# Kernel optimization log

Hardware: AMD Instinct MI355X
Metric: run time of the kernel (lower is better)

The kernel has to match this reference:

```python
import jax, jax.numpy as jnp
import numpy as np

N_NODES = 50000
N_EDGES = 800000
D_IN = 128
HC = 128
D_OUT = 128
BN_EPS = 1e-5
RRELU_SLOPE = (1.0 / 8.0 + 1.0 / 3.0) / 2.0  # RReLU eval mode: (lower+upper)/2 = 11/48


def setup_inputs() -> dict:
    key = jax.random.key(0)
    ks = jax.random.split(key, 10)
    s_in = 1.0 / np.sqrt(D_IN)
    s_hc = 1.0 / np.sqrt(HC)
    return {
        "x": jax.random.normal(ks[0], (N_NODES, D_IN), jnp.float32),
        "edge_index": jax.random.randint(ks[1], (2, N_EDGES), 0, N_NODES),
        "edge_attr": jax.random.uniform(ks[2], (N_EDGES,), jnp.float32),
        # conv1: GraphConv(D_IN -> HC): lin_rel (with bias) + lin_root (no bias)
        "W1_rel": jax.random.normal(ks[3], (HC, D_IN), jnp.float32) * s_in,
        "b1": jnp.zeros((HC,), jnp.float32),
        "W1_root": jax.random.normal(ks[4], (HC, D_IN), jnp.float32) * s_in,
        # bn1 affine params
        "gamma": jnp.ones((HC,), jnp.float32),
        "beta": jnp.zeros((HC,), jnp.float32),
        # conv2: GraphConv(HC -> D_OUT)
        "W2_rel": jax.random.normal(ks[5], (D_OUT, HC), jnp.float32) * s_hc,
        "b2": jnp.zeros((D_OUT,), jnp.float32),
        "W2_root": jax.random.normal(ks[6], (D_OUT, HC), jnp.float32) * s_hc,
    }


def graph_conv(x, src, tgt, edge_w, W_rel, b_rel, W_root):
    # message: edge_weight * x[src]; aggregate: scatter-add into target nodes
    msg = x[src] * edge_w[:, None]                                   # [E, F]
    agg = jax.ops.segment_sum(msg, tgt, num_segments=x.shape[0])     # [N, F]
    return agg @ W_rel.T + b_rel + x @ W_root.T                      # [N, F_out]


def reference(x, edge_index, edge_attr, W1_rel, b1, W1_root, gamma, beta, W2_rel, b2, W2_root):
    src, tgt = edge_index[0], edge_index[1]
    h = graph_conv(x, src, tgt, edge_attr, W1_rel, b1, W1_root)      # [N, HC]
    # BatchNorm1d (training mode: biased batch stats over node dim)
    mean = h.mean(axis=0)
    var = h.var(axis=0)
    h = (h - mean) * jax.lax.rsqrt(var + BN_EPS) * gamma + beta
    # RReLU (deterministic eval slope)
    h = jnp.where(h >= 0, h, h * RRELU_SLOPE)
    return graph_conv(h, src, tgt, edge_attr, W2_rel, b2, W2_root)   # [N, D_OUT]
```

## Files before the change

kernel.cpp:

```cpp
#include <hip/hip_runtime.h>

#define N_NODES 50000
#define N_EDGES 800000
#define F 128
#define BN_EPS 1e-5f
#define SLOPE 0.22916666666666666f

#define NBKT 196
#define P1_CHUNK 4096
#define P1_EPB 16
#define P1_BLKS 196
#define CASTX_BLKS 6250
#define CASTW_BLKS 64
#define BKT_FINAL_CAP 9984
#define BKT_STRIDE 10240
#define MYR_CAP 18
#define N_RT 3125
#define NPART 8

typedef __attribute__((ext_vector_type(8))) short bf16x8;
typedef __attribute__((ext_vector_type(4))) float f32x4;
typedef unsigned long long u64;

__device__ __forceinline__ float bf2f(ushort u) {
    union { uint i; float f; } v; v.i = (uint)u << 16; return v.f;
}
__device__ __forceinline__ ushort f2bf(float f) {
    union { float f; uint i; } v; v.f = f;
    uint r = v.i + 0x7fffu + ((v.i >> 16) & 1u);
    return (ushort)(r >> 16);
}

__global__ __launch_bounds__(256) void s1p_k(const int* __restrict__ src,
        const int* __restrict__ tgt, const float* __restrict__ ew,
        u64* __restrict__ stg, int* __restrict__ cntM, int* __restrict__ offM,
        const float* __restrict__ x, ushort* __restrict__ xb,
        const float* __restrict__ W1r, const float* __restrict__ W1t,
        const float* __restrict__ W2r, const float* __restrict__ W2t,
        ushort* __restrict__ wb) {
    const int b = blockIdx.x;
    if (b >= P1_BLKS) {
        if (b < P1_BLKS + CASTX_BLKS) {
            int i = (b - P1_BLKS) * 256 + threadIdx.x;
            float4 v = reinterpret_cast<const float4*>(x)[i];
            ushort4 o;
            o.x = f2bf(v.x); o.y = f2bf(v.y); o.z = f2bf(v.z); o.w = f2bf(v.w);
            reinterpret_cast<ushort4*>(xb)[i] = o;
        } else {
            int i = (b - P1_BLKS - CASTX_BLKS) * 256 + threadIdx.x;
            int m = i >> 12;
            int j = i & 4095;
            const float* sp = (m == 0) ? W1r : (m == 1) ? W1t : (m == 2) ? W2r : W2t;
            float4 v = reinterpret_cast<const float4*>(sp)[j];
            ushort4 o;
            o.x = f2bf(v.x); o.y = f2bf(v.y); o.z = f2bf(v.z); o.w = f2bf(v.w);
            reinterpret_cast<ushort4*>(wb)[i] = o;
        }
        return;
    }
    __shared__ uint cnt[256];
    __shared__ uint base[256];
    __shared__ uint lcur[256];
    __shared__ u64 lrec[P1_CHUNK];

    const int e0 = b * P1_CHUNK;
    const int nE = min(P1_CHUNK, N_EDGES - e0);
    cnt[threadIdx.x] = 0;
    __syncthreads();

    u64 myrec[P1_EPB];
    bool myok[P1_EPB];
#pragma unroll
    for (int k = 0; k < P1_EPB; ++k) {
        int idx = threadIdx.x + (k << 8);
        bool ok = idx < nE;
        myok[k] = ok;
        if (ok) {
            int e = e0 + idx;
            uint t = (uint)tgt[e];
            uint lo = (uint)(ushort)src[e] | ((uint)f2bf(ew[e]) << 16);
            myrec[k] = (u64)lo | ((u64)t << 32);
            atomicAdd(&cnt[t >> 8], 1u);
        }
    }
    __syncthreads();
    uint v = cnt[threadIdx.x];
    base[threadIdx.x] = v;
    __syncthreads();
    for (int o = 1; o < 256; o <<= 1) {
        uint t = (threadIdx.x >= (unsigned)o) ? base[threadIdx.x - o] : 0;
        __syncthreads();
        base[threadIdx.x] += t;
        __syncthreads();
    }
    uint excl = base[threadIdx.x] - v;
    lcur[threadIdx.x] = excl;
    if (threadIdx.x < NBKT) {
        cntM[threadIdx.x * NBKT + b] = (int)v;
        offM[threadIdx.x * NBKT + b] = (int)excl;
    }
    __syncthreads();
#pragma unroll
    for (int k = 0; k < P1_EPB; ++k) {
        if (myok[k]) {
            uint bb = (uint)(myrec[k] >> 40);
            uint slot = atomicAdd(&lcur[bb], 1u);
            lrec[slot] = myrec[k];
        }
    }
    __syncthreads();
    for (int s = threadIdx.x; s < nE; s += 256)
        stg[(size_t)b * P1_CHUNK + s] = lrec[s];
}

__global__ __launch_bounds__(256) void sort2_k(const int* __restrict__ cntM,
        const int* __restrict__ offM, const u64* __restrict__ stg,
        uint* __restrict__ recs, int2* __restrict__ rng,
        float* __restrict__ Sp, float* __restrict__ S2p) {
    __shared__ int soff[256];
    __shared__ int astart[256];
    __shared__ int lcnt[256];
    __shared__ int lcur[256];
    __shared__ int sc[256];
    __shared__ int tot_s;
    __shared__ uint lrec[BKT_FINAL_CAP];
    const int B = blockIdx.x;
    const int tid = threadIdx.x;

    if (B < NPART && tid < 128) {
        Sp[B * 128 + tid] = 0.f;
        S2p[B * 128 + tid] = 0.f;
    }

    int c = (tid < NBKT) ? cntM[B * NBKT + tid] : 0;
    soff[tid] = (tid < NBKT) ? offM[B * NBKT + tid] : 0;
    sc[tid] = c;
    lcnt[tid] = 0;
    __syncthreads();
    for (int o = 1; o < 256; o <<= 1) {
        int t = (tid >= o) ? sc[tid - o] : 0;
        __syncthreads();
        sc[tid] += t;
        __syncthreads();
    }
    astart[tid] = sc[tid] - c;
    if (tid == 255) tot_s = sc[255];
    __syncthreads();
    const int tot = tot_s;

    u64 myr[MYR_CAP];
#pragma unroll
    for (int k = 0; k < MYR_CAP; ++k) {
        int i = tid + (k << 8);
        if (i < tot) {
            int lo = 0, hi = NBKT - 1;
            while (lo < hi) {
                int mid = (lo + hi + 1) >> 1;
                if (astart[mid] <= i) lo = mid; else hi = mid - 1;
            }
            int j = i - astart[lo];
            u64 r = stg[(size_t)lo * P1_CHUNK + soff[lo] + j];
            myr[k] = r;
            atomicAdd(&lcnt[(int)(r >> 32) & 255], 1);
        }
    }
    __syncthreads();
    const int node = B * 256 + tid;
    int myc = lcnt[tid];
    int myp = (myc + 7) & ~7;
    if (node >= N_NODES) myp = 0;
    sc[tid] = myp;
    __syncthreads();
    for (int o = 1; o < 256; o <<= 1) {
        int t = (tid >= o) ? sc[tid - o] : 0;
        __syncthreads();
        sc[tid] += t;
        __syncthreads();
    }
    const int myoff = sc[tid] - myp;
    const int ptot = sc[255];
    lcur[tid] = myoff;
    const int fbase = B * BKT_STRIDE;
    if (node < N_NODES) rng[node] = make_int2(fbase + myoff, fbase + myoff + myp);
    for (int i = tid; i < ptot; i += 256) lrec[i] = 0;
    __syncthreads();
#pragma unroll
    for (int k = 0; k < MYR_CAP; ++k) {
        int i = tid + (k << 8);
        if (i < tot) {
            u64 r = myr[k];
            int n = (int)(r >> 32) & 255;
            int p = atomicAdd(&lcur[n], 1);
            lrec[p] = (uint)r;
        }
    }
    __syncthreads();
    for (int i = tid; i < ptot; i += 256) recs[fbase + i] = lrec[i];
}

template <int LAYER>
__global__ __launch_bounds__(256) void fused_k(
        const ushort* __restrict__ featb, const int2* __restrict__ rng,
        const uint* __restrict__ recs, const ushort* __restrict__ Wr,
        const ushort* __restrict__ Wt, const float* __restrict__ bias,
        const float* __restrict__ gamma, const float* __restrict__ beta,
        float* __restrict__ Sp, float* __restrict__ S2p,
        ushort* __restrict__ outh, float* __restrict__ outf) {
    __shared__ __align__(16) uint aggu[16 * 64];
    __shared__ __align__(16) float scs[128];
    __shared__ __align__(16) float shs[128];

    const int tid = threadIdx.x;
    const int lane = tid & 63;
    const int wave = tid >> 6;
    const int row0 = blockIdx.x * 16;

    if (LAYER == 2) {
        if (tid < 128) {
            float s = 0.f, q = 0.f;
#pragma unroll
            for (int p = 0; p < NPART; ++p) {
                s += Sp[p * 128 + tid];
                q += S2p[p * 128 + tid];
            }
            float mean = s * (1.f / N_NODES);
            float var = q * (1.f / N_NODES) - mean * mean;
            float inv = rsqrtf(var + BN_EPS);
            float sc = gamma[tid] * inv;
            scs[tid] = sc;
            shs[tid] = beta[tid] - mean * sc;
        }
        __syncthreads();
    }

    const int lane2 = lane * 2;
    float lsc0 = 1.f, lsh0 = 0.f, lsc1 = 1.f, lsh1 = 0.f;
    if (LAYER == 2) {
        lsc0 = scs[lane2]; lsh0 = shs[lane2];
        lsc1 = scs[lane2 + 1]; lsh1 = shs[lane2 + 1];
    }

#pragma unroll
    for (int i = 0; i < 4; ++i) {
        const int r = wave * 4 + i;
        const int2 rr = rng[row0 + r];
        float a0 = 0.f, a1 = 0.f;
        for (int p = rr.x; p < rr.y; p += 8) {
            uint4 ra = *reinterpret_cast<const uint4*>(recs + p);
            uint4 rb = *reinterpret_cast<const uint4*>(recs + p + 4);
            uint u0 = *reinterpret_cast<const uint*>(featb + (size_t)(ra.x & 0xffffu) * F + lane2);
            uint u1 = *reinterpret_cast<const uint*>(featb + (size_t)(ra.y & 0xffffu) * F + lane2);
            uint u2 = *reinterpret_cast<const uint*>(featb + (size_t)(ra.z & 0xffffu) * F + lane2);
            uint u3 = *reinterpret_cast<const uint*>(featb + (size_t)(ra.w & 0xffffu) * F + lane2);
            uint u4 = *reinterpret_cast<const uint*>(featb + (size_t)(rb.x & 0xffffu) * F + lane2);
            uint u5 = *reinterpret_cast<const uint*>(featb + (size_t)(rb.y & 0xffffu) * F + lane2);
            uint u6 = *reinterpret_cast<const uint*>(featb + (size_t)(rb.z & 0xffffu) * F + lane2);
            uint u7 = *reinterpret_cast<const uint*>(featb + (size_t)(rb.w & 0xffffu) * F + lane2);
            float w0 = bf2f((ushort)(ra.x >> 16)), w1 = bf2f((ushort)(ra.y >> 16));
            float w2 = bf2f((ushort)(ra.z >> 16)), w3 = bf2f((ushort)(ra.w >> 16));
            float w4 = bf2f((ushort)(rb.x >> 16)), w5 = bf2f((ushort)(rb.y >> 16));
            float w6 = bf2f((ushort)(rb.z >> 16)), w7 = bf2f((ushort)(rb.w >> 16));
            auto proc = [&](uint u, float w) {
                float t0 = bf2f((ushort)u);
                float t1 = bf2f((ushort)(u >> 16));
                if (LAYER == 2) {
                    t0 = t0 * lsc0 + lsh0; t0 = fmaxf(t0, t0 * SLOPE);
                    t1 = t1 * lsc1 + lsh1; t1 = fmaxf(t1, t1 * SLOPE);
                }
                a0 += w * t0;
                a1 += w * t1;
            };
            proc(u0, w0); proc(u1, w1); proc(u2, w2); proc(u3, w3);
            proc(u4, w4); proc(u5, w5); proc(u6, w6); proc(u7, w7);
        }
        aggu[(r * 64 + lane) ^ ((r & 7) << 2)] =
            (uint)f2bf(a0) | ((uint)f2bf(a1) << 16);
    }
    __syncthreads();

    const int quad = lane >> 4;
    const int l16 = lane & 15;
    const int cb = wave * 32;
    const float bias0 = bias[cb + l16];
    const float bias1 = bias[cb + 16 + l16];

    f32x4 acc0 = {0.f, 0.f, 0.f, 0.f};
    f32x4 acc1 = {0.f, 0.f, 0.f, 0.f};

#pragma unroll
    for (int s = 0; s < 4; ++s) {
        const int k0 = s * 32 + quad * 8;
        const int ai = (l16 * 64 + (k0 >> 1)) ^ ((l16 & 7) << 2);
        bf16x8 aR = *reinterpret_cast<const bf16x8*>(&aggu[ai]);
        bf16x8 w0 = *reinterpret_cast<const bf16x8*>(Wr + (cb + l16) * F + k0);
        bf16x8 w1 = *reinterpret_cast<const bf16x8*>(Wr + (cb + 16 + l16) * F + k0);
        acc0 = __builtin_amdgcn_mfma_f32_16x16x32_bf16(aR, w0, acc0, 0, 0, 0);
        acc1 = __builtin_amdgcn_mfma_f32_16x16x32_bf16(aR, w1, acc1, 0, 0, 0);
    }
#pragma unroll
    for (int s = 0; s < 4; ++s) {
        const int k0 = s * 32 + quad * 8;
        bf16x8 aT = *reinterpret_cast<const bf16x8*>(featb + (size_t)(row0 + l16) * F + k0);
        if (LAYER == 2) {
#pragma unroll
            for (int e = 0; e < 8; ++e) {
                float t = bf2f((ushort)aT[e]) * scs[k0 + e] + shs[k0 + e];
                t = fmaxf(t, t * SLOPE);
                aT[e] = (short)f2bf(t);
            }
        }
        bf16x8 w0 = *reinterpret_cast<const bf16x8*>(Wt + (cb + l16) * F + k0);
        bf16x8 w1 = *reinterpret_cast<const bf16x8*>(Wt + (cb + 16 + l16) * F + k0);
        acc0 = __builtin_amdgcn_mfma_f32_16x16x32_bf16(aT, w0, acc0, 0, 0, 0);
        acc1 = __builtin_amdgcn_mfma_f32_16x16x32_bf16(aT, w1, acc1, 0, 0, 0);
    }

    const int rbase = row0 + quad * 4;
    if (LAYER == 1) {
        float s0 = 0.f, q0 = 0.f, s1 = 0.f, q1 = 0.f;
#pragma unroll
        for (int g = 0; g < 4; ++g) {
            float v0 = acc0[g] + bias0;
            float v1 = acc1[g] + bias1;
            outh[(size_t)(rbase + g) * F + cb + l16] = f2bf(v0);
            outh[(size_t)(rbase + g) * F + cb + 16 + l16] = f2bf(v1);
            s0 += v0; q0 += v0 * v0;
            s1 += v1; q1 += v1 * v1;
        }
        s0 += __shfl_down(s0, 32); s0 += __shfl_down(s0, 16);
        q0 += __shfl_down(q0, 32); q0 += __shfl_down(q0, 16);
        s1 += __shfl_down(s1, 32); s1 += __shfl_down(s1, 16);
        q1 += __shfl_down(q1, 32); q1 += __shfl_down(q1, 16);
        if (lane < 16) {
            float* Sb = Sp + (size_t)(blockIdx.x & (NPART - 1)) * 128;
            float* S2b = S2p + (size_t)(blockIdx.x & (NPART - 1)) * 128;
            unsafeAtomicAdd(&Sb[cb + lane], s0);
            unsafeAtomicAdd(&S2b[cb + lane], q0);
            unsafeAtomicAdd(&Sb[cb + 16 + lane], s1);
            unsafeAtomicAdd(&S2b[cb + 16 + lane], q1);
        }
    } else {
#pragma unroll
        for (int g = 0; g < 4; ++g) {
            outf[(size_t)(rbase + g) * F + cb + l16] = acc0[g] + bias0;
            outf[(size_t)(rbase + g) * F + cb + 16 + l16] = acc1[g] + bias1;
        }
    }
}

extern "C" void kernel_launch(void* const* d_in, const int* in_sizes, int n_in,
                              void* d_out, int out_size, void* d_ws, size_t ws_size,
                              hipStream_t stream) {
    const float* x     = (const float*)d_in[0];
    const int*   ei    = (const int*)d_in[1];
    const float* ea    = (const float*)d_in[2];
    const float* W1r   = (const float*)d_in[3];
    const float* b1    = (const float*)d_in[4];
    const float* W1t   = (const float*)d_in[5];
    const float* gamma = (const float*)d_in[6];
    const float* beta  = (const float*)d_in[7];
    const float* W2r   = (const float*)d_in[8];
    const float* b2    = (const float*)d_in[9];
    const float* W2t   = (const float*)d_in[10];
    float* out = (float*)d_out;

    char* ws = (char*)d_ws;
    size_t off = 0;
    ushort* featb = (ushort*)(ws + off); off += (size_t)N_NODES * F * 2;
    ushort* hraw  = (ushort*)(ws + off); off += (size_t)N_NODES * F * 2;
    u64*    stg   = (u64*)(ws + off);    off += (size_t)P1_BLKS * P1_CHUNK * 8;
    uint*   recs  = (uint*)(ws + off);   off += (size_t)NBKT * BKT_STRIDE * 4;
    int*    cntM  = (int*)(ws + off);    off += (size_t)NBKT * NBKT * 4;
    int*    offM  = (int*)(ws + off);    off += (size_t)NBKT * NBKT * 4;
    int2*   rng   = (int2*)(ws + off);   off += (size_t)N_NODES * 8;
    ushort* wb    = (ushort*)(ws + off); off += 4 * 16384 * 2;
    float*  Sp    = (float*)(ws + off);  off += NPART * 128 * 4;
    float*  S2p   = (float*)(ws + off);  off += NPART * 128 * 4;

    const int* srcp = ei;
    const int* tgtp = ei + N_EDGES;

    s1p_k<<<P1_BLKS + CASTX_BLKS + CASTW_BLKS, 256, 0, stream>>>(
        srcp, tgtp, ea, stg, cntM, offM, x, featb, W1r, W1t, W2r, W2t, wb);
    sort2_k<<<NBKT, 256, 0, stream>>>(cntM, offM, stg, recs, rng, Sp, S2p);

    fused_k<1><<<N_RT, 256, 0, stream>>>(featb, rng, recs, wb, wb + 16384, b1,
                                         gamma, beta, Sp, S2p, hraw, out);
    fused_k<2><<<N_RT, 256, 0, stream>>>(hraw, rng, recs, wb + 32768, wb + 49152, b2,
                                         gamma, beta, Sp, S2p, hraw, out);
}
```

Baseline: 233.3 us.

## Fuse second-stage edge sort into layer-1 aggregation kernel per row tile

Removes the separate per-bucket sort kernel. Each layer-1 tile block now re-reads its bucket's staged edge records, filters the edges targeting its 16 rows, and builds a CSR slice in shared memory that it aggregates from directly. It also writes that slice to global memory for layer 2. BN stat zeroing moves into an extra block of the first kernel. This saves a launch and a global round trip, but every bucket is now scanned redundantly by 16 blocks.

After: 235.6 us. No clear change (+1.0%).

```diff
diff --git a/kernel.cpp b/kernel.cpp
--- a/kernel.cpp
+++ b/kernel.cpp
@@ -12,9 +12,8 @@
 #define P1_BLKS 196
 #define CASTX_BLKS 6250
 #define CASTW_BLKS 64
-#define BKT_FINAL_CAP 9984
-#define BKT_STRIDE 10240
-#define MYR_CAP 18
+#define KSC 18
+#define CREC_STRIDE 512
 #define N_RT 3125
 #define NPART 8
 
@@ -37,7 +36,7 @@
         const float* __restrict__ x, ushort* __restrict__ xb,
         const float* __restrict__ W1r, const float* __restrict__ W1t,
         const float* __restrict__ W2r, const float* __restrict__ W2t,
-        ushort* __restrict__ wb) {
+        ushort* __restrict__ wb, float* __restrict__ SpZ) {
     const int b = blockIdx.x;
     if (b >= P1_BLKS) {
         if (b < P1_BLKS + CASTX_BLKS) {
@@ -46,7 +45,7 @@
             ushort4 o;
             o.x = f2bf(v.x); o.y = f2bf(v.y); o.z = f2bf(v.z); o.w = f2bf(v.w);
             reinterpret_cast<ushort4*>(xb)[i] = o;
-        } else {
+        } else if (b < P1_BLKS + CASTX_BLKS + CASTW_BLKS) {
             int i = (b - P1_BLKS - CASTX_BLKS) * 256 + threadIdx.x;
             int m = i >> 12;
             int j = i & 4095;
@@ -55,6 +54,8 @@
             ushort4 o;
             o.x = f2bf(v.x); o.y = f2bf(v.y); o.z = f2bf(v.z); o.w = f2bf(v.w);
             reinterpret_cast<ushort4*>(wb)[i] = o;
+        } else {
+            for (int i = threadIdx.x; i < 2 * NPART * 128; i += 256) SpZ[i] = 0.f;
         }
         return;
     }
@@ -113,107 +114,31 @@
         stg[(size_t)b * P1_CHUNK + s] = lrec[s];
 }
 
-__global__ __launch_bounds__(256) void sort2_k(const int* __restrict__ cntM,
-        const int* __restrict__ offM, const u64* __restrict__ stg,
-        uint* __restrict__ recs, int2* __restrict__ rng,
-        float* __restrict__ Sp, float* __restrict__ S2p) {
-    __shared__ int soff[256];
-    __shared__ int astart[256];
-    __shared__ int lcnt[256];
-    __shared__ int lcur[256];
-    __shared__ int sc[256];
-    __shared__ int tot_s;
-    __shared__ uint lrec[BKT_FINAL_CAP];
-    const int B = blockIdx.x;
-    const int tid = threadIdx.x;
-
-    if (B < NPART && tid < 128) {
-        Sp[B * 128 + tid] = 0.f;
-        S2p[B * 128 + tid] = 0.f;
-    }
-
-    int c = (tid < NBKT) ? cntM[B * NBKT + tid] : 0;
-    soff[tid] = (tid < NBKT) ? offM[B * NBKT + tid] : 0;
-    sc[tid] = c;
-    lcnt[tid] = 0;
-    __syncthreads();
-    for (int o = 1; o < 256; o <<= 1) {
-        int t = (tid >= o) ? sc[tid - o] : 0;
-        __syncthreads();
-        sc[tid] += t;
-        __syncthreads();
-    }
-    astart[tid] = sc[tid] - c;
-    if (tid == 255) tot_s = sc[255];
-    __syncthreads();
-    const int tot = tot_s;
-
-    u64 myr[MYR_CAP];
-#pragma unroll
-    for (int k = 0; k < MYR_CAP; ++k) {
-        int i = tid + (k << 8);
-        if (i < tot) {
-            int lo = 0, hi = NBKT - 1;
-            while (lo < hi) {
-                int mid = (lo + hi + 1) >> 1;
-                if (astart[mid] <= i) lo = mid; else hi = mid - 1;
-            }
-            int j = i - astart[lo];
-            u64 r = stg[(size_t)lo * P1_CHUNK + soff[lo] + j];
-            myr[k] = r;
-            atomicAdd(&lcnt[(int)(r >> 32) & 255], 1);
-        }
-    }
-    __syncthreads();
-    const int node = B * 256 + tid;
-    int myc = lcnt[tid];
-    int myp = (myc + 7) & ~7;
-    if (node >= N_NODES) myp = 0;
-    sc[tid] = myp;
-    __syncthreads();
-    for (int o = 1; o < 256; o <<= 1) {
-        int t = (tid >= o) ? sc[tid - o] : 0;
-        __syncthreads();
-        sc[tid] += t;
-        __syncthreads();
-    }
-    const int myoff = sc[tid] - myp;
-    const int ptot = sc[255];
-    lcur[tid] = myoff;
-    const int fbase = B * BKT_STRIDE;
-    if (node < N_NODES) rng[node] = make_int2(fbase + myoff, fbase + myoff + myp);
-    for (int i = tid; i < ptot; i += 256) lrec[i] = 0;
-    __syncthreads();
-#pragma unroll
-    for (int k = 0; k < MYR_CAP; ++k) {
-        int i = tid + (k << 8);
-        if (i < tot) {
-            u64 r = myr[k];
-            int n = (int)(r >> 32) & 255;
-            int p = atomicAdd(&lcur[n], 1);
-            lrec[p] = (uint)r;
-        }
-    }
-    __syncthreads();
-    for (int i = tid; i < ptot; i += 256) recs[fbase + i] = lrec[i];
-}
-
 template <int LAYER>
 __global__ __launch_bounds__(256) void fused_k(
-        const ushort* __restrict__ featb, const int2* __restrict__ rng,
-        const uint* __restrict__ recs, const ushort* __restrict__ Wr,
-        const ushort* __restrict__ Wt, const float* __restrict__ bias,
-        const float* __restrict__ gamma, const float* __restrict__ beta,
-        float* __restrict__ Sp, float* __restrict__ S2p,
-        ushort* __restrict__ outh, float* __restrict__ outf) {
+        const ushort* __restrict__ featb, int2* __restrict__ rng,
+        uint* __restrict__ crecs, const u64* __restrict__ stg,
+        const int* __restrict__ cntM, const int* __restrict__ offM,
+        const ushort* __restrict__ Wr, const ushort* __restrict__ Wt,
+        const float* __restrict__ bias, const float* __restrict__ gamma,
+        const float* __restrict__ beta, float* __restrict__ Sp,
+        float* __restrict__ S2p, ushort* __restrict__ outh,
+        float* __restrict__ outf) {
     __shared__ __align__(16) uint aggu[16 * 64];
     __shared__ __align__(16) float scs[128];
     __shared__ __align__(16) float shs[128];
+    __shared__ int sc[256];
+    __shared__ int soff[256];
+    __shared__ int astart[256];
+    __shared__ int lcnt16[16], lcur16[16], p4s[16], nstart[17];
+    __shared__ int tot_s;
+    __shared__ __align__(16) uint lrec[CREC_STRIDE];
 
     const int tid = threadIdx.x;
     const int lane = tid & 63;
     const int wave = tid >> 6;
-    const int row0 = blockIdx.x * 16;
+    const int t = blockIdx.x;
+    const int row0 = t * 16;
 
     if (LAYER == 2) {
         if (tid < 128) {
@@ -226,11 +151,81 @@
             float mean = s * (1.f / N_NODES);
             float var = q * (1.f / N_NODES) - mean * mean;
             float inv = rsqrtf(var + BN_EPS);
-            float sc = gamma[tid] * inv;
-            scs[tid] = sc;
-            shs[tid] = beta[tid] - mean * sc;
-        }
-        __syncthreads();
+            float scv = gamma[tid] * inv;
+            scs[tid] = scv;
+            shs[tid] = beta[tid] - mean * scv;
+        }
+        __syncthreads();
+    }
+
+    if (LAYER == 1) {
+        const int B = t >> 4;
+        int c = (tid < NBKT) ? cntM[B * NBKT + tid] : 0;
+        soff[tid] = (tid < NBKT) ? offM[B * NBKT + tid] : 0;
+        sc[tid] = c;
+        if (tid < 16) lcnt16[tid] = 0;
+        __syncthreads();
+        for (int o = 1; o < 256; o <<= 1) {
+            int tv = (tid >= o) ? sc[tid - o] : 0;
+            __syncthreads();
+            sc[tid] += tv;
+            __syncthreads();
+        }
+        astart[tid] = sc[tid] - c;
+        if (tid == 255) tot_s = sc[255];
+        __syncthreads();
+        const int tot = tot_s;
+
+        u64 myr[KSC];
+#pragma unroll
+        for (int k = 0; k < KSC; ++k) {
+            int i = tid + (k << 8);
+            u64 r = ~0ull;
+            if (i < tot) {
+                int lo = 0;
+#pragma unroll
+                for (int st = 128; st; st >>= 1) {
+                    int cand = lo + st;
+                    if (cand < NBKT && astart[cand] <= i) lo = cand;
+                }
+                int j = i - astart[lo];
+                r = stg[(size_t)lo * P1_CHUNK + soff[lo] + j];
+                uint tg = (uint)(r >> 32);
+                if ((int)(tg >> 4) == t) atomicAdd(&lcnt16[tg & 15u], 1);
+            }
+            myr[k] = r;
+        }
+        __syncthreads();
+        if (tid == 0) {
+            int run = 0;
+#pragma unroll
+            for (int n = 0; n < 16; ++n) {
+                nstart[n] = run;
+                int p = (lcnt16[n] + 7) & ~7;
+                p4s[n] = p;
+                run += p;
+            }
+            nstart[16] = run;
+        }
+        __syncthreads();
+        const int ptot = nstart[16];
+        if (tid < 16) lcur16[tid] = nstart[tid];
+        for (int i = tid; i < ptot; i += 256) lrec[i] = 0;
+        __syncthreads();
+#pragma unroll
+        for (int k = 0; k < KSC; ++k) {
+            u64 r = myr[k];
+            uint tg = (uint)(r >> 32);
+            if ((int)(tg >> 4) == t) {
+                int p = atomicAdd(&lcur16[tg & 15u], 1);
+                lrec[p] = (uint)r;
+            }
+        }
+        __syncthreads();
+        for (int i = tid; i < ptot; i += 256) crecs[t * CREC_STRIDE + i] = lrec[i];
+        if (tid < 16)
+            rng[row0 + tid] = make_int2(t * CREC_STRIDE + nstart[tid],
+                                        t * CREC_STRIDE + nstart[tid] + p4s[tid]);
     }
 
     const int lane2 = lane * 2;
@@ -243,11 +238,19 @@
 #pragma unroll
     for (int i = 0; i < 4; ++i) {
         const int r = wave * 4 + i;
-        const int2 rr = rng[row0 + r];
         float a0 = 0.f, a1 = 0.f;
-        for (int p = rr.x; p < rr.y; p += 8) {
-            uint4 ra = *reinterpret_cast<const uint4*>(recs + p);
-            uint4 rb = *reinterpret_cast<const uint4*>(recs + p + 4);
+        int p, pe;
+        if (LAYER == 1) { p = nstart[r]; pe = p + p4s[r]; }
+        else { int2 rr = rng[row0 + r]; p = rr.x; pe = rr.y; }
+        for (; p < pe; p += 8) {
+            uint4 ra, rb;
+            if (LAYER == 1) {
+                ra = *reinterpret_cast<const uint4*>(&lrec[p]);
+                rb = *reinterpret_cast<const uint4*>(&lrec[p + 4]);
+            } else {
+                ra = *reinterpret_cast<const uint4*>(crecs + p);
+                rb = *reinterpret_cast<const uint4*>(crecs + p + 4);
+            }
             uint u0 = *reinterpret_cast<const uint*>(featb + (size_t)(ra.x & 0xffffu) * F + lane2);
             uint u1 = *reinterpret_cast<const uint*>(featb + (size_t)(ra.y & 0xffffu) * F + lane2);
             uint u2 = *reinterpret_cast<const uint*>(featb + (size_t)(ra.z & 0xffffu) * F + lane2);
@@ -304,9 +307,9 @@
         if (LAYER == 2) {
 #pragma unroll
             for (int e = 0; e < 8; ++e) {
-                float t = bf2f((ushort)aT[e]) * scs[k0 + e] + shs[k0 + e];
-                t = fmaxf(t, t * SLOPE);
-                aT[e] = (short)f2bf(t);
+                float tv = bf2f((ushort)aT[e]) * scs[k0 + e] + shs[k0 + e];
+                tv = fmaxf(tv, tv * SLOPE);
+                aT[e] = (short)f2bf(tv);
             }
         }
         bf16x8 w0 = *reinterpret_cast<const bf16x8*>(Wt + (cb + l16) * F + k0);
@@ -369,7 +372,7 @@
     ushort* featb = (ushort*)(ws + off); off += (size_t)N_NODES * F * 2;
     ushort* hraw  = (ushort*)(ws + off); off += (size_t)N_NODES * F * 2;
     u64*    stg   = (u64*)(ws + off);    off += (size_t)P1_BLKS * P1_CHUNK * 8;
-    uint*   recs  = (uint*)(ws + off);   off += (size_t)NBKT * BKT_STRIDE * 4;
+    uint*   crecs = (uint*)(ws + off);   off += (size_t)N_RT * CREC_STRIDE * 4;
     int*    cntM  = (int*)(ws + off);    off += (size_t)NBKT * NBKT * 4;
     int*    offM  = (int*)(ws + off);    off += (size_t)NBKT * NBKT * 4;
     int2*   rng   = (int2*)(ws + off);   off += (size_t)N_NODES * 8;
@@ -380,12 +383,13 @@
     const int* srcp = ei;
     const int* tgtp = ei + N_EDGES;
 
-    s1p_k<<<P1_BLKS + CASTX_BLKS + CASTW_BLKS, 256, 0, stream>>>(
-        srcp, tgtp, ea, stg, cntM, offM, x, featb, W1r, W1t, W2r, W2t, wb);
-    sort2_k<<<NBKT, 256, 0, stream>>>(cntM, offM, stg, recs, rng, Sp, S2p);
-
-    fused_k<1><<<N_RT, 256, 0, stream>>>(featb, rng, recs, wb, wb + 16384, b1,
-                                         gamma, beta, Sp, S2p, hraw, out);
-    fused_k<2><<<N_RT, 256, 0, stream>>>(hraw, rng, recs, wb + 32768, wb + 49152, b2,
-                                         gamma, beta, Sp, S2p, hraw, out);
-}
+    s1p_k<<<P1_BLKS + CASTX_BLKS + CASTW_BLKS + 1, 256, 0, stream>>>(
+        srcp, tgtp, ea, stg, cntM, offM, x, featb, W1r, W1t, W2r, W2t, wb, Sp);
+
+    fused_k<1><<<N_RT, 256, 0, stream>>>(featb, rng, crecs, stg, cntM, offM,
+                                         wb, wb + 16384, b1, gamma, beta,
+                                         Sp, S2p, hraw, out);
+    fused_k<2><<<N_RT, 256, 0, stream>>>(hraw, rng, crecs, stg, cntM, offM,
+                                         wb + 32768, wb + 49152, b2, gamma, beta,
+                                         Sp, S2p, hraw, out);
+}
```
